# Performance work log

Measured on AMD Instinct MI355X. Metric: run time of the kernel, lower is better.

The kernel has to match this reference:

```python
import jax, jax.numpy as jnp
import numpy as np

B, S, H = 32, 2048, 512

def setup_inputs() -> dict:
    key = jax.random.key(0)
    k1, k2, k3, k4 = jax.random.split(key, 4)
    Y = jax.random.normal(k1, (B, S, H), dtype=jnp.float32)
    mask_Y = jnp.ones((B, S), dtype=jnp.float32)
    W = jax.random.normal(k2, (H, H), dtype=jnp.float32)
    b = jax.random.normal(k3, (H,), dtype=jnp.float32)
    w = jax.random.normal(k4, (H,), dtype=jnp.float32)
    return {"Y": Y, "mask_Y": mask_Y, "W": W, "b": b, "w": w}

def reference(Y, mask_Y, W, b, w):
    # u: [B,S,H] = tanh(Y @ W + b)
    u = jnp.tanh(jnp.einsum('bsh,hd->bsd', Y, W) + b)
    # scores: [B,S] = u . w, masked with large negative additive bias
    scores = jnp.einsum('bsh,h->bs', u, w) - 1000.0 * (1.0 - mask_Y)
    alpha = jax.nn.softmax(scores, axis=1)  # [B,S]
    # c_star: [B,H] = attention-weighted sum of Y
    c_star = jnp.einsum('bs,bsh->bh', alpha, Y)
    return c_star
```

## Files before the change

kernel.cpp:

```cpp
#include <hip/hip_runtime.h>
#include <hip/hip_bf16.h>


#define Bsz 32
#define Ssz 2048
#define Hsz 512
#define Msz (Bsz * Ssz)

using half8  = __attribute__((ext_vector_type(8))) _Float16;
using half4v = __attribute__((ext_vector_type(4))) _Float16;
using floatx4 = __attribute__((ext_vector_type(4))) float;

__device__ __forceinline__ void llds(_Float16* l, const _Float16* g) {
  __builtin_amdgcn_global_load_lds((const __attribute__((address_space(1))) void*)g,
                                   (__attribute__((address_space(3))) void*)l, 16, 0, 0);
}

__device__ __forceinline__ float fast_tanh(float x) {
  const float e = __expf(2.f * x);
  return 1.f - 2.f / (e + 1.f);
}

__global__ __launch_bounds__(256) void wsplit_k(const float* __restrict__ W,
                                                _Float16* __restrict__ Wt) {
  __shared__ float tile[32][33];
  const int bx = blockIdx.x & 15, by = blockIdx.x >> 4;
  const int tx = threadIdx.x & 31, ty = threadIdx.x >> 5;
#pragma unroll
  for (int i = 0; i < 4; ++i)
    tile[ty + 8 * i][tx] = W[(size_t)(by * 32 + ty + 8 * i) * Hsz + bx * 32 + tx];
  __syncthreads();
#pragma unroll
  for (int i = 0; i < 4; ++i) {
    const int n = bx * 32 + ty + 8 * i;
    const int k = by * 32 + tx;
    const float v = tile[tx][ty + 8 * i];
    const _Float16 hi = (_Float16)v;
    const _Float16 lo = (_Float16)(v - (float)hi);
    Wt[(size_t)n * 1024 + k] = hi;
    Wt[(size_t)n * 1024 + 512 + k] = lo;
  }
}

__global__ __launch_bounds__(256) void yconv_k(const float4* __restrict__ Y4,
                                               half4v* __restrict__ Y16v) {
  const size_t i = (size_t)blockIdx.x * 256 + threadIdx.x;
  const float4 v = Y4[i];
  half4v h;
  h[0] = (_Float16)v.x; h[1] = (_Float16)v.y; h[2] = (_Float16)v.z; h[3] = (_Float16)v.w;
  Y16v[i] = h;
}

__global__ __launch_bounds__(256) void gemm_score_k(const _Float16* __restrict__ Y16,
                                                    const _Float16* __restrict__ Wt,
                                                    const float* __restrict__ bvec,
                                                    const float* __restrict__ wvec,
                                                    float* __restrict__ scores) {
  __shared__ __align__(16) _Float16 As[128 * 32];
  __shared__ __align__(16) _Float16 Bh[128 * 32];
  __shared__ __align__(16) _Float16 Bl[128 * 32];
  const int tid = threadIdx.x;
  const int lane = tid & 63, wv = tid >> 6;
  const int wr = wv >> 1, wc = wv & 1;
  const int lr = lane & 15, lq = lane >> 4;
  const int mblk = blockIdx.x >> 2, nblk = blockIdx.x & 3;

  floatx4 acc[4][4];
#pragma unroll
  for (int rf = 0; rf < 4; ++rf)
#pragma unroll
    for (int cf = 0; cf < 4; ++cf)
      acc[rf][cf] = (floatx4){0.f, 0.f, 0.f, 0.f};

  const size_t arow0 = (size_t)mblk * 128 * 512;
  const size_t brow0 = (size_t)nblk * 128 * 1024;

  for (int it = 0; it < 16; ++it) {
    const int k0 = it * 32;
#pragma unroll
    for (int i = 0; i < 2; ++i) {
      const int cbase = i * 256 + wv * 64;
      const int c = cbase + lane;
      const int row = c >> 2, part = c & 3;
      const _Float16* ga = Y16 + arow0 + (size_t)row * 512 + (k0 + part * 8);
      const _Float16* gb = Wt + brow0 + (size_t)row * 1024 + (k0 + part * 8);
      llds(&As[cbase * 8], ga);
      llds(&Bh[cbase * 8], gb);
      llds(&Bl[cbase * 8], gb + 512);
    }
    __syncthreads();

    half8 a[4], bhf[4], blf[4];
#pragma unroll
    for (int rf = 0; rf < 4; ++rf)
      a[rf] = *(const half8*)&As[(wr * 64 + rf * 16 + lr) * 32 + lq * 8];
#pragma unroll
    for (int cf = 0; cf < 4; ++cf) {
      const int n = (wc * 64 + cf * 16 + lr) * 32 + lq * 8;
      bhf[cf] = *(const half8*)&Bh[n];
      blf[cf] = *(const half8*)&Bl[n];
    }
#pragma unroll
    for (int rf = 0; rf < 4; ++rf)
#pragma unroll
      for (int cf = 0; cf < 4; ++cf)
        acc[rf][cf] = __builtin_amdgcn_mfma_f32_16x16x32_f16(a[rf], bhf[cf], acc[rf][cf], 0, 0, 0);
#pragma unroll
    for (int rf = 0; rf < 4; ++rf)
#pragma unroll
      for (int cf = 0; cf < 4; ++cf)
        acc[rf][cf] = __builtin_amdgcn_mfma_f32_16x16x32_f16(a[rf], blf[cf], acc[rf][cf], 0, 0, 0);
    __syncthreads();
  }

  float bb[4], ww[4];
  const int colbase = nblk * 128 + wc * 64;
#pragma unroll
  for (int cf = 0; cf < 4; ++cf) {
    const int col = colbase + cf * 16 + lr;
    bb[cf] = bvec[col];
    ww[cf] = wvec[col];
  }
  const int rowbase = mblk * 128 + wr * 64;
#pragma unroll
  for (int rf = 0; rf < 4; ++rf) {
#pragma unroll
    for (int r = 0; r < 4; ++r) {
      float v = 0.f;
#pragma unroll
      for (int cf = 0; cf < 4; ++cf)
        v += fast_tanh(acc[rf][cf][r] + bb[cf]) * ww[cf];
      v += __shfl_xor(v, 1, 16);
      v += __shfl_xor(v, 2, 16);
      v += __shfl_xor(v, 4, 16);
      v += __shfl_xor(v, 8, 16);
      if (lr == 0)
        atomicAdd(&scores[rowbase + rf * 16 + lq * 4 + r], v);
    }
  }
}

__global__ __launch_bounds__(256) void softmax_k(const float* __restrict__ scores,
                                                 const float* __restrict__ mask,
                                                 float* __restrict__ alpha) {
  const int b = blockIdx.x, t = threadIdx.x;
  const int lane = t & 63, wv = t >> 6;
  float s[8];
  float mx = -3.4e38f;
#pragma unroll
  for (int i = 0; i < 8; ++i) {
    const int idx = b * Ssz + i * 256 + t;
    const float v = scores[idx] - 1000.f * (1.f - mask[idx]);
    s[i] = v;
    mx = fmaxf(mx, v);
  }
  for (int off = 32; off > 0; off >>= 1) mx = fmaxf(mx, __shfl_xor(mx, off, 64));
  __shared__ float rm[4], rs[4];
  if (lane == 0) rm[wv] = mx;
  __syncthreads();
  mx = fmaxf(fmaxf(rm[0], rm[1]), fmaxf(rm[2], rm[3]));
  float sum = 0.f;
#pragma unroll
  for (int i = 0; i < 8; ++i) {
    s[i] = __expf(s[i] - mx);
    sum += s[i];
  }
  for (int off = 32; off > 0; off >>= 1) sum += __shfl_xor(sum, off, 64);
  if (lane == 0) rs[wv] = sum;
  __syncthreads();
  sum = rs[0] + rs[1] + rs[2] + rs[3];
  const float inv = 1.f / sum;
#pragma unroll
  for (int i = 0; i < 8; ++i) alpha[b * Ssz + i * 256 + t] = s[i] * inv;
}

__global__ __launch_bounds__(256) void wsum_k(const float* __restrict__ alpha,
                                              const float* __restrict__ Y,
                                              float* __restrict__ out) {
  const int b = blockIdx.x >> 4, sc = blockIdx.x & 15;
  const int t = threadIdx.x;
  const float2* Y2 = (const float2*)(Y + ((size_t)b * Ssz + sc * 128) * Hsz);
  const float* al = alpha + b * Ssz + sc * 128;
  float cx = 0.f, cy = 0.f;
  for (int s = 0; s < 128; ++s) {
    const float a = al[s];
    const float2 y = Y2[(size_t)s * 256 + t];
    cx = fmaf(a, y.x, cx);
    cy = fmaf(a, y.y, cy);
  }
  atomicAdd(&out[b * Hsz + 2 * t], cx);
  atomicAdd(&out[b * Hsz + 2 * t + 1], cy);
}

extern "C" void kernel_launch(void* const* d_in, const int* in_sizes, int n_in,
                              void* d_out, int out_size, void* d_ws, size_t ws_size,
                              hipStream_t stream) {
  (void)in_sizes; (void)n_in; (void)out_size; (void)ws_size;
  const float* Y    = (const float*)d_in[0];
  const float* mask = (const float*)d_in[1];
  const float* W    = (const float*)d_in[2];
  const float* bvec = (const float*)d_in[3];
  const float* wvec = (const float*)d_in[4];
  float* out = (float*)d_out;

  char* ws = (char*)d_ws;
  _Float16* Y16 = (_Float16*)ws;
  _Float16* Wt  = (_Float16*)(ws + ((size_t)64 << 20));
  float* scores = (float*)(ws + ((size_t)65 << 20));
  float* alpha  = (float*)(ws + ((size_t)65 << 20) + (256u << 10));

  hipMemsetAsync(scores, 0, Msz * sizeof(float), stream);
  hipMemsetAsync(out, 0, Bsz * Hsz * sizeof(float), stream);

  wsplit_k<<<256, 256, 0, stream>>>(W, Wt);
  yconv_k<<<(Msz * Hsz / 4) / 256, 256, 0, stream>>>((const float4*)Y, (half4v*)Y16);
  gemm_score_k<<<(Msz / 128) * 4, 256, 0, stream>>>(Y16, Wt, bvec, wvec, scores);
  softmax_k<<<Bsz, 256, 0, stream>>>(scores, mask, alpha);
  wsum_k<<<Bsz * 16, 256, 0, stream>>>(alpha, Y, out);
}
```

Baseline: 318.2 us.

## Fuse fp32-to-fp16 Y conversion into GEMM, swizzle LDS, drop score atomics

Removes the separate Y conversion kernel and its fp16 intermediate by loading fp32 Y in the GEMM and converting in registers before storing to LDS. LDS layout is XOR-swizzled to cut bank conflicts, and block indices are remapped so the four N-blocks sharing an M-tile run near each other for L2 reuse. Score atomics and their memset are replaced by per-N-block partial buffers that the softmax sums, and the weighted-sum kernel uses four times more blocks. A-tile loads now go through registers rather than direct-to-LDS loads, which may add latency.

```diff
diff --git a/kernel.cpp b/kernel.cpp
--- a/kernel.cpp
+++ b/kernel.cpp
@@ -7,8 +7,7 @@
 #define Hsz 512
 #define Msz (Bsz * Ssz)
 
-using half8  = __attribute__((ext_vector_type(8))) _Float16;
-using half4v = __attribute__((ext_vector_type(4))) _Float16;
+using half8   = __attribute__((ext_vector_type(8))) _Float16;
 using floatx4 = __attribute__((ext_vector_type(4))) float;
 
 __device__ __forceinline__ void llds(_Float16* l, const _Float16* g) {
@@ -42,20 +41,11 @@
   }
 }
 
-__global__ __launch_bounds__(256) void yconv_k(const float4* __restrict__ Y4,
-                                               half4v* __restrict__ Y16v) {
-  const size_t i = (size_t)blockIdx.x * 256 + threadIdx.x;
-  const float4 v = Y4[i];
-  half4v h;
-  h[0] = (_Float16)v.x; h[1] = (_Float16)v.y; h[2] = (_Float16)v.z; h[3] = (_Float16)v.w;
-  Y16v[i] = h;
-}
-
-__global__ __launch_bounds__(256) void gemm_score_k(const _Float16* __restrict__ Y16,
+__global__ __launch_bounds__(256) void gemm_score_k(const float* __restrict__ Y,
                                                     const _Float16* __restrict__ Wt,
                                                     const float* __restrict__ bvec,
                                                     const float* __restrict__ wvec,
-                                                    float* __restrict__ scores) {
+                                                    float* __restrict__ scores4) {
   __shared__ __align__(16) _Float16 As[128 * 32];
   __shared__ __align__(16) _Float16 Bh[128 * 32];
   __shared__ __align__(16) _Float16 Bl[128 * 32];
@@ -63,7 +53,10 @@
   const int lane = tid & 63, wv = tid >> 6;
   const int wr = wv >> 1, wc = wv & 1;
   const int lr = lane & 15, lq = lane >> 4;
-  const int mblk = blockIdx.x >> 2, nblk = blockIdx.x & 3;
+  const int g = blockIdx.x;
+  const int x = g & 7, q = g >> 3;
+  const int nblk = q & 3;
+  const int mblk = (q >> 2) * 8 + x;
 
   floatx4 acc[4][4];
 #pragma unroll
@@ -72,7 +65,11 @@
     for (int cf = 0; cf < 4; ++cf)
       acc[rf][cf] = (floatx4){0.f, 0.f, 0.f, 0.f};
 
-  const size_t arow0 = (size_t)mblk * 128 * 512;
+  const int arow = tid >> 1;
+  const int p0 = (tid & 1) * 2;
+  const float* aga = Y + ((size_t)(mblk * 128 + arow)) * Hsz + p0 * 8;
+  const int s0 = (p0 ^ ((arow >> 1) & 3)) * 8;
+  const int s1 = ((p0 + 1) ^ ((arow >> 1) & 3)) * 8;
   const size_t brow0 = (size_t)nblk * 128 * 1024;
 
   for (int it = 0; it < 16; ++it) {
@@ -81,24 +78,37 @@
     for (int i = 0; i < 2; ++i) {
       const int cbase = i * 256 + wv * 64;
       const int c = cbase + lane;
-      const int row = c >> 2, part = c & 3;
-      const _Float16* ga = Y16 + arow0 + (size_t)row * 512 + (k0 + part * 8);
-      const _Float16* gb = Wt + brow0 + (size_t)row * 1024 + (k0 + part * 8);
-      llds(&As[cbase * 8], ga);
+      const int brow = c >> 2;
+      const int gpart = (c & 3) ^ ((c >> 3) & 3);
+      const _Float16* gb = Wt + brow0 + (size_t)brow * 1024 + (k0 + gpart * 8);
       llds(&Bh[cbase * 8], gb);
       llds(&Bl[cbase * 8], gb + 512);
     }
+    {
+      const float4* g4 = (const float4*)(aga + k0);
+      const float4 f0 = g4[0], f1 = g4[1], f2 = g4[2], f3 = g4[3];
+      half8 h0, h1;
+      h0[0] = (_Float16)f0.x; h0[1] = (_Float16)f0.y; h0[2] = (_Float16)f0.z; h0[3] = (_Float16)f0.w;
+      h0[4] = (_Float16)f1.x; h0[5] = (_Float16)f1.y; h0[6] = (_Float16)f1.z; h0[7] = (_Float16)f1.w;
+      h1[0] = (_Float16)f2.x; h1[1] = (_Float16)f2.y; h1[2] = (_Float16)f2.z; h1[3] = (_Float16)f2.w;
+      h1[4] = (_Float16)f3.x; h1[5] = (_Float16)f3.y; h1[6] = (_Float16)f3.z; h1[7] = (_Float16)f3.w;
+      *(half8*)&As[arow * 32 + s0] = h0;
+      *(half8*)&As[arow * 32 + s1] = h1;
+    }
     __syncthreads();
 
     half8 a[4], bhf[4], blf[4];
 #pragma unroll
-    for (int rf = 0; rf < 4; ++rf)
-      a[rf] = *(const half8*)&As[(wr * 64 + rf * 16 + lr) * 32 + lq * 8];
+    for (int rf = 0; rf < 4; ++rf) {
+      const int ar = wr * 64 + rf * 16 + lr;
+      a[rf] = *(const half8*)&As[ar * 32 + (lq ^ ((ar >> 1) & 3)) * 8];
+    }
 #pragma unroll
     for (int cf = 0; cf < 4; ++cf) {
-      const int n = (wc * 64 + cf * 16 + lr) * 32 + lq * 8;
-      bhf[cf] = *(const half8*)&Bh[n];
-      blf[cf] = *(const half8*)&Bl[n];
+      const int nr = wc * 64 + cf * 16 + lr;
+      const int na = nr * 32 + (lq ^ ((nr >> 1) & 3)) * 8;
+      bhf[cf] = *(const half8*)&Bh[na];
+      blf[cf] = *(const half8*)&Bl[na];
     }
 #pragma unroll
     for (int rf = 0; rf < 4; ++rf)
@@ -121,7 +131,7 @@
     bb[cf] = bvec[col];
     ww[cf] = wvec[col];
   }
-  const int rowbase = mblk * 128 + wr * 64;
+  float* red = (float*)As;
 #pragma unroll
   for (int rf = 0; rf < 4; ++rf) {
 #pragma unroll
@@ -135,12 +145,15 @@
       v += __shfl_xor(v, 4, 16);
       v += __shfl_xor(v, 8, 16);
       if (lr == 0)
-        atomicAdd(&scores[rowbase + rf * 16 + lq * 4 + r], v);
-    }
-  }
-}
-
-__global__ __launch_bounds__(256) void softmax_k(const float* __restrict__ scores,
+        red[(wr * 64 + rf * 16 + lq * 4 + r) * 2 + wc] = v;
+    }
+  }
+  __syncthreads();
+  if (tid < 128)
+    scores4[(size_t)nblk * Msz + mblk * 128 + tid] = red[2 * tid] + red[2 * tid + 1];
+}
+
+__global__ __launch_bounds__(256) void softmax_k(const float* __restrict__ scores4,
                                                  const float* __restrict__ mask,
                                                  float* __restrict__ alpha) {
   const int b = blockIdx.x, t = threadIdx.x;
@@ -150,7 +163,8 @@
 #pragma unroll
   for (int i = 0; i < 8; ++i) {
     const int idx = b * Ssz + i * 256 + t;
-    const float v = scores[idx] - 1000.f * (1.f - mask[idx]);
+    float v = scores4[idx] + scores4[Msz + idx] + scores4[2 * Msz + idx] + scores4[3 * Msz + idx];
+    v -= 1000.f * (1.f - mask[idx]);
     s[i] = v;
     mx = fmaxf(mx, v);
   }
@@ -177,12 +191,12 @@
 __global__ __launch_bounds__(256) void wsum_k(const float* __restrict__ alpha,
                                               const float* __restrict__ Y,
                                               float* __restrict__ out) {
-  const int b = blockIdx.x >> 4, sc = blockIdx.x & 15;
+  const int b = blockIdx.x >> 6, sc = blockIdx.x & 63;
   const int t = threadIdx.x;
-  const float2* Y2 = (const float2*)(Y + ((size_t)b * Ssz + sc * 128) * Hsz);
-  const float* al = alpha + b * Ssz + sc * 128;
+  const float2* Y2 = (const float2*)(Y + ((size_t)b * Ssz + sc * 32) * Hsz);
+  const float* al = alpha + b * Ssz + sc * 32;
   float cx = 0.f, cy = 0.f;
-  for (int s = 0; s < 128; ++s) {
+  for (int s = 0; s < 32; ++s) {
     const float a = al[s];
     const float2 y = Y2[(size_t)s * 256 + t];
     cx = fmaf(a, y.x, cx);
@@ -204,17 +218,14 @@
   float* out = (float*)d_out;
 
   char* ws = (char*)d_ws;
-  _Float16* Y16 = (_Float16*)ws;
-  _Float16* Wt  = (_Float16*)(ws + ((size_t)64 << 20));
-  float* scores = (float*)(ws + ((size_t)65 << 20));
-  float* alpha  = (float*)(ws + ((size_t)65 << 20) + (256u << 10));
-
-  hipMemsetAsync(scores, 0, Msz * sizeof(float), stream);
+  _Float16* Wt   = (_Float16*)ws;
+  float* scores4 = (float*)(ws + ((size_t)1 << 20));
+  float* alpha   = (float*)(ws + ((size_t)2 << 20));
+
   hipMemsetAsync(out, 0, Bsz * Hsz * sizeof(float), stream);
 
   wsplit_k<<<256, 256, 0, stream>>>(W, Wt);
-  yconv_k<<<(Msz * Hsz / 4) / 256, 256, 0, stream>>>((const float4*)Y, (half4v*)Y16);
-  gemm_score_k<<<(Msz / 128) * 4, 256, 0, stream>>>(Y16, Wt, bvec, wvec, scores);
-  softmax_k<<<Bsz, 256, 0, stream>>>(scores, mask, alpha);
-  wsum_k<<<Bsz * 16, 256, 0, stream>>>(alpha, Y, out);
-}
+  gemm_score_k<<<(Msz / 128) * 4, 256, 0, stream>>>(Y, Wt, bvec, wvec, scores4);
+  softmax_k<<<Bsz, 256, 0, stream>>>(scores4, mask, alpha);
+  wsum_k<<<Bsz * 64, 256, 0, stream>>>(alpha, Y, out);
+}
```

Result: faster. 289.3 us (-9.1%).
